# Kernel tuning notes

Measured on AMD Instinct MI355X. Metric: run time of the kernel, lower is better.

## Reference

```python
import jax, jax.numpy as jnp
import numpy as np

H = 1024        # hidden_size
I = 2048        # intermediate_size
E = 8           # num_experts
K = 2           # num_experts_per_tok
AUX_COEF = 0.01
Z_COEF = 0.001


def setup_inputs() -> dict:
    key = jax.random.key(0)
    ks = jax.random.split(key, 8)
    s = 0.02
    return {
        "hidden_states": jax.random.normal(ks[0], (1, 2048, H), dtype=jnp.float32),
        "router_w": jax.random.normal(ks[1], (H, E), dtype=jnp.float32) * s,
        "eg": jax.random.normal(ks[2], (E, H, I), dtype=jnp.float32) * s,  # gate_proj per expert
        "eu": jax.random.normal(ks[3], (E, H, I), dtype=jnp.float32) * s,  # up_proj per expert
        "ed": jax.random.normal(ks[4], (E, I, H), dtype=jnp.float32) * s,  # down_proj per expert
        "sg": jax.random.normal(ks[5], (H, I), dtype=jnp.float32) * s,     # shared expert gate
        "su": jax.random.normal(ks[6], (H, I), dtype=jnp.float32) * s,     # shared expert up
        "sd": jax.random.normal(ks[7], (I, H), dtype=jnp.float32) * s,     # shared expert down
    }


def reference(hidden_states, router_w, eg, eu, ed, sg, su, sd):
    B, S, _ = hidden_states.shape
    x = hidden_states.reshape(-1, H)  # [T, H]

    # shared expert (num_shared_experts = 1)
    shared = (jax.nn.silu(x @ sg) * (x @ su)) @ sd  # [T, H]

    # router: linear -> softmax -> top-k, renormalize top-k probs
    logits = x @ router_w                      # [T, E]
    probs = jax.nn.softmax(logits, axis=-1)
    topw, topi = jax.lax.top_k(probs, K)       # [T, K]
    topw = topw / jnp.sum(topw, axis=-1, keepdims=True)

    # combine weights [T, E]: weight of expert e for token t (0 if not routed)
    combine = jnp.sum(jax.nn.one_hot(topi, E, dtype=x.dtype) * topw[..., None], axis=1)

    # dense expert compute (mathematically identical to masked gather/scatter loop)
    g = jnp.einsum('th,ehi->eti', x, eg)       # [E, T, I]
    u = jnp.einsum('th,ehi->eti', x, eu)
    h = jax.nn.silu(g) * u
    expert_out = jnp.einsum('eti,eih->eth', h, ed)  # [E, T, H]
    routed = jnp.einsum('eth,te->th', expert_out, combine)

    output = (shared + routed).reshape(B, S, H)

    # aux losses: Switch-style load balancing + router z-loss
    f = jnp.mean(jax.nn.one_hot(topi, E, dtype=x.dtype), axis=(0, 1))  # fraction dispatched
    p = jnp.mean(probs, axis=0)                                        # mean router prob
    lb_loss = AUX_COEF * E * jnp.sum(f * p)
    z_loss = Z_COEF * jnp.mean(jax.nn.logsumexp(logits, axis=-1) ** 2)
    aux_loss = lb_loss + z_loss
    return output, aux_loss
```

## Files before the change

### kernel.cpp

```cpp
#include <hip/hip_runtime.h>
#include <hip/hip_bf16.h>
#include <stdint.h>

#define T_ 2048
#define H_ 1024
#define I_ 2048
#define E_ 8
#define NE_ 9

typedef __attribute__((ext_vector_type(8))) short bf16x8;
typedef __attribute__((ext_vector_type(4))) float f32x4;

__device__ __forceinline__ unsigned short f2bf(float f) {
  unsigned int u; __builtin_memcpy(&u, &f, 4);
  u = (u + 0x7fffu + ((u >> 16) & 1u)) >> 16;
  return (unsigned short)u;
}
__device__ __forceinline__ void cvt2(float a, float b, unsigned short* dst) {
  __hip_bfloat162 h = __float22bfloat162_rn(float2{a, b});
  __builtin_memcpy(dst, &h, 4);
}
__device__ __forceinline__ void gll16(const void* g, void* l) {
  __builtin_amdgcn_global_load_lds((const __attribute__((address_space(1))) void*)g,
                                   (__attribute__((address_space(3))) void*)l, 16, 0, 0);
}

__global__ __launch_bounds__(256) void k_pack(
    const float* __restrict__ eg, const float* __restrict__ eu, const float* __restrict__ ed,
    const float* __restrict__ sg, const float* __restrict__ su, const float* __restrict__ sd,
    unsigned short* __restrict__ wgp, unsigned short* __restrict__ wup,
    unsigned short* __restrict__ wdp) {
  int kt = blockIdx.x, nt = blockIdx.y, z = blockIdx.z;
  int grp = z / NE_, e = z % NE_;
  int K = (grp == 2) ? I_ : H_;
  int N = (grp == 2) ? H_ : I_;
  if (kt * 32 >= K || nt * 64 >= N) return;
  const float* src; unsigned short* dst;
  if (grp == 0)      { src = (e < E_) ? eg + (size_t)e * H_ * I_ : sg; dst = wgp + (size_t)e * H_ * I_; }
  else if (grp == 1) { src = (e < E_) ? eu + (size_t)e * H_ * I_ : su; dst = wup + (size_t)e * H_ * I_; }
  else               { src = (e < E_) ? ed + (size_t)e * I_ * H_ : sd; dst = wdp + (size_t)e * I_ * H_; }
  int t = threadIdx.x;
  int q = t >> 6, nn = t & 63;
  int k0 = kt * 32 + q * 8, n = nt * 64 + nn;
  unsigned short o[8];
#pragma unroll
  for (int j = 0; j < 8; j += 2) {
    float a = src[(size_t)(k0 + j) * N + n];
    float b = src[(size_t)(k0 + j + 1) * N + n];
    cvt2(a, b, &o[j]);
  }
  size_t tile = ((size_t)nt * (K / 32) + kt) * 2048;
  *(bf16x8*)&dst[tile + q * 512 + nn * 8] = *(bf16x8*)o;
}

__global__ __launch_bounds__(256) void k_router(
    const float* __restrict__ x, const float* __restrict__ rw,
    int* __restrict__ topi, float* __restrict__ topw,
    float* __restrict__ probs, float* __restrict__ lse2) {
  __shared__ float lrw[E_ * H_];
  int tid = threadIdx.x;
#pragma unroll
  for (int i = 0; i < 8; i++) {
    int idx = i * 256 + tid;
    float4 v = ((const float4*)rw)[idx];
    int f = idx * 4; int h = f >> 3; int e0 = f & 7;
    lrw[(e0 + 0) * H_ + h] = v.x;
    lrw[(e0 + 1) * H_ + h] = v.y;
    lrw[(e0 + 2) * H_ + h] = v.z;
    lrw[(e0 + 3) * H_ + h] = v.w;
  }
  __syncthreads();
  int w = tid >> 6, lane = tid & 63;
  int t = blockIdx.x * 4 + w;
  const float* xp = x + (size_t)t * H_ + lane;
  float xr[16];
#pragma unroll
  for (int j = 0; j < 16; j++) xr[j] = xp[j * 64];
  float acc[E_];
#pragma unroll
  for (int e = 0; e < E_; e++) acc[e] = 0.f;
#pragma unroll
  for (int j = 0; j < 16; j++) {
    float xf = xr[j];
    const float* wp = &lrw[j * 64 + lane];
#pragma unroll
    for (int e = 0; e < E_; e++) acc[e] += xf * wp[e * H_];
  }
#pragma unroll
  for (int off = 32; off >= 1; off >>= 1) {
#pragma unroll
    for (int e = 0; e < E_; e++) acc[e] += __shfl_xor(acc[e], off, 64);
  }
  if (lane == 0) {
    float m = acc[0];
#pragma unroll
    for (int e = 1; e < E_; e++) m = fmaxf(m, acc[e]);
    float p[E_], s = 0.f;
#pragma unroll
    for (int e = 0; e < E_; e++) { p[e] = expf(acc[e] - m); s += p[e]; }
    float inv = 1.f / s;
#pragma unroll
    for (int e = 0; e < E_; e++) p[e] *= inv;
    float lse = m + logf(s);
    lse2[t] = lse * lse;
    float4 p0 = {p[0], p[1], p[2], p[3]}, p1 = {p[4], p[5], p[6], p[7]};
    ((float4*)(probs + t * 8))[0] = p0;
    ((float4*)(probs + t * 8))[1] = p1;
    int i0 = 0;
#pragma unroll
    for (int e = 1; e < E_; e++) if (p[e] > p[i0]) i0 = e;
    int i1 = (i0 == 0) ? 1 : 0;
#pragma unroll
    for (int e = 0; e < E_; e++) if (e != i0 && e != i1 && p[e] > p[i1]) i1 = e;
    float w0 = p[i0], w1 = p[i1], wsum = w0 + w1;
    topi[t * 2] = i0; topi[t * 2 + 1] = i1;
    topw[t * 2] = w0 / wsum; topw[t * 2 + 1] = w1 / wsum;
  }
}

__global__ __launch_bounds__(256) void k_reduce(
    const float* __restrict__ probs, const float* __restrict__ lse2,
    const int* __restrict__ topi,
    int* cnt, int* poffs, float* out_aux) {
  __shared__ float sp[256][9];
  __shared__ int sc[256][8];
  int tid = threadIdx.x;
  float ps[9] = {0.f, 0.f, 0.f, 0.f, 0.f, 0.f, 0.f, 0.f, 0.f};
  int c[8] = {0, 0, 0, 0, 0, 0, 0, 0};
  for (int t = tid; t < T_; t += 256) {
#pragma unroll
    for (int e = 0; e < E_; e++) ps[e] += probs[t * 8 + e];
    ps[8] += lse2[t];
    c[topi[t * 2]]++; c[topi[t * 2 + 1]]++;
  }
#pragma unroll
  for (int e = 0; e < 9; e++) sp[tid][e] = ps[e];
#pragma unroll
  for (int e = 0; e < 8; e++) sc[tid][e] = c[e];
  __syncthreads();
  for (int s = 128; s > 0; s >>= 1) {
    if (tid < s) {
#pragma unroll
      for (int e = 0; e < 9; e++) sp[tid][e] += sp[tid + s][e];
#pragma unroll
      for (int e = 0; e < 8; e++) sc[tid][e] += sc[tid + s][e];
    }
    __syncthreads();
  }
  if (tid == 0) {
#pragma unroll
    for (int e = 0; e < E_; e++) cnt[e] = sc[0][e];
    cnt[E_] = T_;
    int po = 0;
    for (int e = 0; e < NE_; e++) { poffs[e] = po; po += ((cnt[e] + 127) >> 7) << 7; }
    poffs[NE_] = po;
    float lb = 0.f;
#pragma unroll
    for (int e = 0; e < E_; e++)
      lb += ((float)cnt[e] / 4096.f) * (sp[0][e] / 2048.f);
    out_aux[0] = 0.01f * 8.f * lb + 0.001f * (sp[0][8] / 2048.f);
  }
}

__global__ __launch_bounds__(256) void k_fill(
    const int* __restrict__ topi, const float* __restrict__ topw,
    const int* __restrict__ poffs, int* cur, int* tok, float* wgt) {
  __shared__ int hist[8];
  __shared__ int base[8];
  int tid = threadIdx.x;
  int t = blockIdx.x * 256 + tid;
  if (tid < 8) hist[tid] = 0;
  __syncthreads();
  int e0 = topi[t * 2], e1 = topi[t * 2 + 1];
  int p0 = atomicAdd(&hist[e0], 1);
  int p1 = atomicAdd(&hist[e1], 1);
  __syncthreads();
  if (tid < 8) base[tid] = atomicAdd(&cur[tid], hist[tid]);
  __syncthreads();
  tok[poffs[e0] + base[e0] + p0] = t; wgt[poffs[e0] + base[e0] + p0] = topw[t * 2];
  tok[poffs[e1] + base[e1] + p1] = t; wgt[poffs[e1] + base[e1] + p1] = topw[t * 2 + 1];
  int p8 = poffs[E_];
  tok[p8 + t] = t;
  wgt[p8 + t] = 1.f;
}

__global__ __launch_bounds__(256) void k_packA(
    const float* __restrict__ x, const int* __restrict__ cnt,
    const int* __restrict__ poffs, const int* __restrict__ tok,
    unsigned short* __restrict__ apack) {
  int kc = blockIdx.x, mt = blockIdx.y, e = blockIdx.z;
  int cnt_e = cnt[e];
  if (mt * 128 >= cnt_e) return;
  int po = poffs[e];
  int rt = (po >> 7) + mt;
  int t = threadIdx.x;
  int m = t & 127, qh = t >> 7;
  int atok = tok[po + min(mt * 128 + m, cnt_e - 1)];
  const float* arow = x + (size_t)atok * H_;
  size_t abase = (size_t)rt * 32 * 4096;
#pragma unroll
  for (int ki = 0; ki < 4; ki++) {
    int kt = kc * 4 + ki;
#pragma unroll
    for (int qo = 0; qo < 2; qo++) {
      int q = qh + qo * 2;
      const float* s = arow + kt * 32 + q * 8;
      float4 v0 = *(const float4*)s, v1 = *(const float4*)(s + 4);
      unsigned short t8[8];
      cvt2(v0.x, v0.y, t8); cvt2(v0.z, v0.w, t8 + 2);
      cvt2(v1.x, v1.y, t8 + 4); cvt2(v1.z, v1.w, t8 + 6);
      *(bf16x8*)&apack[abase + (size_t)kt * 4096 + q * 1024 + m * 8] = *(bf16x8*)t8;
    }
  }
}

#define G1_GRID 1792
__global__ __launch_bounds__(256) void k_gemm1(
    const unsigned short* __restrict__ apack,
    const unsigned short* __restrict__ wgp, const unsigned short* __restrict__ wup,
    const int* __restrict__ cnt, const int* __restrict__ poffs,
    unsigned short* __restrict__ hbuf) {
  int lin = blockIdx.x;
  int s = (lin & 7) * (G1_GRID / 8) + (lin >> 3);
  int rt = s >> 5, nt = s & 31;
  int rtTotal = poffs[NE_] >> 7;
  if (rt >= rtTotal) return;
  int ro = rt << 7;
  int e = 0;
#pragma unroll
  for (int i = 1; i < NE_; i++) if (poffs[i] <= ro) e = i;
  int po = poffs[e];
  int cnt_e = cnt[e];
  int mt = (ro - po) >> 7;

  __shared__ __align__(16) unsigned short As[2][4096];
  __shared__ __align__(16) unsigned short BgS[2][2048];
  __shared__ __align__(16) unsigned short BuS[2][2048];

  int tid = threadIdx.x;
  int lane = tid & 63, w = tid >> 6;
  int quad = lane >> 4, l15 = lane & 15;
  int wm = w >> 1, wn = w & 1;

  const unsigned short* abase = apack + (size_t)rt * 32 * 4096;
  const unsigned short* bgb = wgp + (size_t)e * H_ * I_ + (size_t)nt * 32 * 2048;
  const unsigned short* bub = wup + (size_t)e * H_ * I_ + (size_t)nt * 32 * 2048;

  f32x4 zero = {0.f, 0.f, 0.f, 0.f};
  f32x4 accg[4][2], accu[4][2];
#pragma unroll
  for (int mi = 0; mi < 4; mi++)
#pragma unroll
    for (int ni = 0; ni < 2; ni++) { accg[mi][ni] = zero; accu[mi][ni] = zero; }

#define STAGE1(kt, b) do { \
    const unsigned short* asrc = abase + (size_t)(kt) * 4096 + w * 1024 + lane * 8; \
    gll16(asrc, &As[b][w * 1024]); \
    gll16(asrc + 512, &As[b][w * 1024 + 512]); \
    gll16(bgb + (size_t)(kt) * 2048 + w * 512 + lane * 8, &BgS[b][w * 512]); \
    gll16(bub + (size_t)(kt) * 2048 + w * 512 + lane * 8, &BuS[b][w * 512]); \
  } while (0)

  STAGE1(0, 0);
  __syncthreads();
  for (int kt = 0; kt < 32; kt++) {
    int cur = kt & 1;
    if (kt < 31) STAGE1(kt + 1, cur ^ 1);
    bf16x8 af[4];
#pragma unroll
    for (int mi = 0; mi < 4; mi++)
      af[mi] = *(const bf16x8*)&As[cur][quad * 1024 + (wm * 64 + mi * 16 + l15) * 8];
#pragma unroll
    for (int ni = 0; ni < 2; ni++) {
      bf16x8 bg = *(const bf16x8*)&BgS[cur][quad * 512 + (wn * 32 + ni * 16 + l15) * 8];
      bf16x8 bu = *(const bf16x8*)&BuS[cur][quad * 512 + (wn * 32 + ni * 16 + l15) * 8];
#pragma unroll
      for (int mi = 0; mi < 4; mi++) {
        accg[mi][ni] = __builtin_amdgcn_mfma_f32_16x16x32_bf16(af[mi], bg, accg[mi][ni], 0, 0, 0);
        accu[mi][ni] = __builtin_amdgcn_mfma_f32_16x16x32_bf16(af[mi], bu, accu[mi][ni], 0, 0, 0);
      }
    }
    __syncthreads();
  }
#undef STAGE1

  size_t hbase = (size_t)rt * 64 * 4096;
  int rem = cnt_e - mt * 128;
#pragma unroll
  for (int ni = 0; ni < 2; ni++) {
    int cc = nt * 64 + wn * 32 + ni * 16 + l15;
    size_t cb = hbase + (size_t)(cc >> 5) * 4096 + (size_t)((cc >> 3) & 3) * 1024 + (cc & 7);
#pragma unroll
    for (int mi = 0; mi < 4; mi++)
#pragma unroll
      for (int r = 0; r < 4; r++) {
        int row = wm * 64 + mi * 16 + quad * 4 + r;
        if (row < rem) {
          float g = accg[mi][ni][r], u = accu[mi][ni][r];
          float sv = g / (1.f + __expf(-g));
          hbuf[cb + (size_t)row * 8] = f2bf(sv * u);
        }
      }
  }
}

#define G2_GRID 896
__global__ __launch_bounds__(256) void k_gemm2(
    const unsigned short* __restrict__ hbuf, const unsigned short* __restrict__ wdp,
    const int* __restrict__ cnt, const int* __restrict__ poffs,
    const int* __restrict__ tok, const float* __restrict__ wgt,
    float* __restrict__ out) {
  int lin = blockIdx.x;
  int s = (lin & 7) * (G2_GRID / 8) + (lin >> 3);
  int rt = s >> 4;
  int r4 = s & 15;
  int nt = r4 >> 1, kh = r4 & 1;
  int rtTotal = poffs[NE_] >> 7;
  if (rt >= rtTotal) return;
  int ro = rt << 7;
  int e = 0;
#pragma unroll
  for (int i = 1; i < NE_; i++) if (poffs[i] <= ro) e = i;
  int po = poffs[e];
  int cnt_e = cnt[e];
  int mt = (ro - po) >> 7;

  __shared__ __align__(16) unsigned short As[2][4096];
  __shared__ __align__(16) unsigned short BdS[2][4096];

  int tid = threadIdx.x;
  int lane = tid & 63, w = tid >> 6;
  int quad = lane >> 4, l15 = lane & 15;
  int wm = w >> 1, wn = w & 1;

  const unsigned short* abase = hbuf + (size_t)rt * 64 * 4096;
  const unsigned short* bb0 = wdp + (size_t)e * I_ * H_ + ((size_t)(2 * nt) * 64) * 2048;
  const unsigned short* bb1 = wdp + (size_t)e * I_ * H_ + ((size_t)(2 * nt + 1) * 64) * 2048;

  f32x4 zero = {0.f, 0.f, 0.f, 0.f};
  f32x4 acc[4][4];
#pragma unroll
  for (int mi = 0; mi < 4; mi++)
#pragma unroll
    for (int ni = 0; ni < 4; ni++) acc[mi][ni] = zero;

#define STAGE2(kt, b) do { \
    const unsigned short* asrc = abase + (size_t)(kt) * 4096 + w * 1024 + lane * 8; \
    gll16(asrc, &As[b][w * 1024]); \
    gll16(asrc + 512, &As[b][w * 1024 + 512]); \
    gll16(bb0 + (size_t)(kt) * 2048 + w * 512 + lane * 8, &BdS[b][w * 512]); \
    gll16(bb1 + (size_t)(kt) * 2048 + w * 512 + lane * 8, &BdS[b][2048 + w * 512]); \
  } while (0)

  int k0 = kh * 32;
  STAGE2(k0, 0);
  __syncthreads();
  for (int kk = 0; kk < 32; kk++) {
    int cur = kk & 1;
    if (kk < 31) STAGE2(k0 + kk + 1, cur ^ 1);
    bf16x8 af[4];
#pragma unroll
    for (int mi = 0; mi < 4; mi++)
      af[mi] = *(const bf16x8*)&As[cur][quad * 1024 + (wm * 64 + mi * 16 + l15) * 8];
#pragma unroll
    for (int ni = 0; ni < 4; ni++) {
      bf16x8 bd = *(const bf16x8*)&BdS[cur][wn * 2048 + quad * 512 + (ni * 16 + l15) * 8];
#pragma unroll
      for (int mi = 0; mi < 4; mi++)
        acc[mi][ni] = __builtin_amdgcn_mfma_f32_16x16x32_bf16(af[mi], bd, acc[mi][ni], 0, 0, 0);
    }
    __syncthreads();
  }
#undef STAGE2

  int rem = cnt_e - mt * 128;
#pragma unroll
  for (int mi = 0; mi < 4; mi++)
#pragma unroll
    for (int r = 0; r < 4; r++) {
      int row = wm * 64 + mi * 16 + quad * 4 + r;
      if (row < rem) {
        int g = po + mt * 128 + row;
        int tt = tok[g];
        float wt = wgt[g];
#pragma unroll
        for (int ni = 0; ni < 4; ni++) {
          int col = nt * 128 + wn * 64 + ni * 16 + l15;
          atomicAdd(&out[(size_t)tt * H_ + col], wt * acc[mi][ni][r]);
        }
      }
    }
}

extern "C" void kernel_launch(void* const* d_in, const int* in_sizes, int n_in,
                              void* d_out, int out_size, void* d_ws, size_t ws_size,
                              hipStream_t stream) {
  const float* x  = (const float*)d_in[0];
  const float* rw = (const float*)d_in[1];
  const float* eg = (const float*)d_in[2];
  const float* eu = (const float*)d_in[3];
  const float* ed = (const float*)d_in[4];
  const float* sg = (const float*)d_in[5];
  const float* su = (const float*)d_in[6];
  const float* sd = (const float*)d_in[7];
  float* out = (float*)d_out;
  char* ws = (char*)d_ws;

  int*   cnt  = (int*)(ws + 64);
  int*   poffs= (int*)(ws + 128);
  int*   cur  = (int*)(ws + 256);
  int*   topi = (int*)(ws + 4096);
  float* topw = (float*)(ws + 4096 + 16384);
  int*   tok  = (int*)(ws + 36864);
  float* wgt  = (float*)(ws + 66560);
  unsigned short* apack = (unsigned short*)(ws + 131072);
  unsigned short* hbuf  = (unsigned short*)(ws + 131072 + 14811136);
  float* probs = (float*)(ws + 44302336);
  float* lse2  = (float*)(ws + 44367872);
  unsigned short* wgp   = (unsigned short*)(ws + 131072 + 14811136 + 29491200);
  unsigned short* wup   = (unsigned short*)((char*)wgp + (size_t)NE_ * H_ * I_ * 2);
  unsigned short* wdp   = (unsigned short*)((char*)wup + (size_t)NE_ * H_ * I_ * 2);

  hipMemsetAsync(ws, 0, 4096, stream);
  hipMemsetAsync(out, 0, (size_t)T_ * H_ * 4, stream);

  dim3 gp(64, 32, 3 * NE_);
  k_pack<<<gp, 256, 0, stream>>>(eg, eu, ed, sg, su, sd, wgp, wup, wdp);
  k_router<<<512, 256, 0, stream>>>(x, rw, topi, topw, probs, lse2);
  k_reduce<<<1, 256, 0, stream>>>(probs, lse2, topi, cnt, poffs, out + (size_t)T_ * H_);
  k_fill<<<8, 256, 0, stream>>>(topi, topw, poffs, cur, tok, wgt);
  dim3 ga(8, 16, NE_);
  k_packA<<<ga, 256, 0, stream>>>(x, cnt, poffs, tok, apack);
  k_gemm1<<<G1_GRID, 256, 0, stream>>>(apack, wgp, wup, cnt, poffs, hbuf);
  k_gemm2<<<G2_GRID, 256, 0, stream>>>(hbuf, wdp, cnt, poffs, tok, wgt, out);
}
```

Before: 428.0 us.

## Fuse pre-GEMM kernels, drop memsets, and coalesce weight pack via LDS

The router kernel now zeroes the output buffer, which replaces both memsets. Reduce and fill are merged into one single-block scheduling kernel that builds the token lists with shared-memory atomics. Weight packing and activation packing are merged into one prep kernel. The weight transpose now reads coalesced float4 rows through an LDS tile instead of strided scalar loads. The goal is fewer launches and better memory coalescing in the weight conversion that dominates pre-GEMM traffic. The cost is a serial single-block fill loop over all tokens.

```diff
diff --git a/kernel.cpp b/kernel.cpp
--- a/kernel.cpp
+++ b/kernel.cpp
@@ -25,40 +25,19 @@
                                    (__attribute__((address_space(3))) void*)l, 16, 0, 0);
 }
 
-__global__ __launch_bounds__(256) void k_pack(
-    const float* __restrict__ eg, const float* __restrict__ eu, const float* __restrict__ ed,
-    const float* __restrict__ sg, const float* __restrict__ su, const float* __restrict__ sd,
-    unsigned short* __restrict__ wgp, unsigned short* __restrict__ wup,
-    unsigned short* __restrict__ wdp) {
-  int kt = blockIdx.x, nt = blockIdx.y, z = blockIdx.z;
-  int grp = z / NE_, e = z % NE_;
-  int K = (grp == 2) ? I_ : H_;
-  int N = (grp == 2) ? H_ : I_;
-  if (kt * 32 >= K || nt * 64 >= N) return;
-  const float* src; unsigned short* dst;
-  if (grp == 0)      { src = (e < E_) ? eg + (size_t)e * H_ * I_ : sg; dst = wgp + (size_t)e * H_ * I_; }
-  else if (grp == 1) { src = (e < E_) ? eu + (size_t)e * H_ * I_ : su; dst = wup + (size_t)e * H_ * I_; }
-  else               { src = (e < E_) ? ed + (size_t)e * I_ * H_ : sd; dst = wdp + (size_t)e * I_ * H_; }
-  int t = threadIdx.x;
-  int q = t >> 6, nn = t & 63;
-  int k0 = kt * 32 + q * 8, n = nt * 64 + nn;
-  unsigned short o[8];
-#pragma unroll
-  for (int j = 0; j < 8; j += 2) {
-    float a = src[(size_t)(k0 + j) * N + n];
-    float b = src[(size_t)(k0 + j + 1) * N + n];
-    cvt2(a, b, &o[j]);
-  }
-  size_t tile = ((size_t)nt * (K / 32) + kt) * 2048;
-  *(bf16x8*)&dst[tile + q * 512 + nn * 8] = *(bf16x8*)o;
-}
-
 __global__ __launch_bounds__(256) void k_router(
     const float* __restrict__ x, const float* __restrict__ rw,
     int* __restrict__ topi, float* __restrict__ topw,
-    float* __restrict__ probs, float* __restrict__ lse2) {
+    float* __restrict__ probs, float* __restrict__ lse2,
+    float* __restrict__ outz) {
+  int tid = threadIdx.x;
+  {
+    float4 zf = {0.f, 0.f, 0.f, 0.f};
+    float4* ob = (float4*)(outz + (size_t)blockIdx.x * 4096);
+#pragma unroll
+    for (int i = 0; i < 4; i++) ob[i * 256 + tid] = zf;
+  }
   __shared__ float lrw[E_ * H_];
-  int tid = threadIdx.x;
 #pragma unroll
   for (int i = 0; i < 8; i++) {
     int idx = i * 256 + tid;
@@ -118,12 +97,15 @@
   }
 }
 
-__global__ __launch_bounds__(256) void k_reduce(
+__global__ __launch_bounds__(256) void k_sched(
     const float* __restrict__ probs, const float* __restrict__ lse2,
-    const int* __restrict__ topi,
-    int* cnt, int* poffs, float* out_aux) {
+    const int* __restrict__ topi, const float* __restrict__ topw,
+    int* cnt, int* poffs, float* out_aux,
+    int* __restrict__ tok, float* __restrict__ wgt) {
   __shared__ float sp[256][9];
   __shared__ int sc[256][8];
+  __shared__ int sbase[NE_];
+  __shared__ int scur[8];
   int tid = threadIdx.x;
   float ps[9] = {0.f, 0.f, 0.f, 0.f, 0.f, 0.f, 0.f, 0.f, 0.f};
   int c[8] = {0, 0, 0, 0, 0, 0, 0, 0};
@@ -152,64 +134,96 @@
     for (int e = 0; e < E_; e++) cnt[e] = sc[0][e];
     cnt[E_] = T_;
     int po = 0;
-    for (int e = 0; e < NE_; e++) { poffs[e] = po; po += ((cnt[e] + 127) >> 7) << 7; }
+    for (int e = 0; e < NE_; e++) {
+      poffs[e] = po; sbase[e] = po;
+      int ce = (e < E_) ? sc[0][e] : T_;
+      po += ((ce + 127) >> 7) << 7;
+    }
     poffs[NE_] = po;
     float lb = 0.f;
 #pragma unroll
     for (int e = 0; e < E_; e++)
-      lb += ((float)cnt[e] / 4096.f) * (sp[0][e] / 2048.f);
+      lb += ((float)sc[0][e] / 4096.f) * (sp[0][e] / 2048.f);
     out_aux[0] = 0.01f * 8.f * lb + 0.001f * (sp[0][8] / 2048.f);
   }
-}
-
-__global__ __launch_bounds__(256) void k_fill(
-    const int* __restrict__ topi, const float* __restrict__ topw,
-    const int* __restrict__ poffs, int* cur, int* tok, float* wgt) {
-  __shared__ int hist[8];
-  __shared__ int base[8];
-  int tid = threadIdx.x;
-  int t = blockIdx.x * 256 + tid;
-  if (tid < 8) hist[tid] = 0;
+  if (tid < 8) scur[tid] = 0;
   __syncthreads();
-  int e0 = topi[t * 2], e1 = topi[t * 2 + 1];
-  int p0 = atomicAdd(&hist[e0], 1);
-  int p1 = atomicAdd(&hist[e1], 1);
-  __syncthreads();
-  if (tid < 8) base[tid] = atomicAdd(&cur[tid], hist[tid]);
-  __syncthreads();
-  tok[poffs[e0] + base[e0] + p0] = t; wgt[poffs[e0] + base[e0] + p0] = topw[t * 2];
-  tok[poffs[e1] + base[e1] + p1] = t; wgt[poffs[e1] + base[e1] + p1] = topw[t * 2 + 1];
-  int p8 = poffs[E_];
-  tok[p8 + t] = t;
-  wgt[p8 + t] = 1.f;
-}
-
-__global__ __launch_bounds__(256) void k_packA(
+  for (int t = tid; t < T_; t += 256) {
+    int e0 = topi[t * 2], e1 = topi[t * 2 + 1];
+    int p0 = atomicAdd(&scur[e0], 1);
+    int p1 = atomicAdd(&scur[e1], 1);
+    tok[sbase[e0] + p0] = t; wgt[sbase[e0] + p0] = topw[t * 2];
+    tok[sbase[e1] + p1] = t; wgt[sbase[e1] + p1] = topw[t * 2 + 1];
+    tok[sbase[E_] + t] = t; wgt[sbase[E_] + t] = 1.f;
+  }
+}
+
+#define PACK_BLKS 27648
+#define PREP_GRID 28800
+__global__ __launch_bounds__(256) void k_prep(
+    const float* __restrict__ eg, const float* __restrict__ eu, const float* __restrict__ ed,
+    const float* __restrict__ sg, const float* __restrict__ su, const float* __restrict__ sd,
+    unsigned short* __restrict__ wgp, unsigned short* __restrict__ wup,
+    unsigned short* __restrict__ wdp,
     const float* __restrict__ x, const int* __restrict__ cnt,
     const int* __restrict__ poffs, const int* __restrict__ tok,
     unsigned short* __restrict__ apack) {
-  int kc = blockIdx.x, mt = blockIdx.y, e = blockIdx.z;
-  int cnt_e = cnt[e];
-  if (mt * 128 >= cnt_e) return;
-  int po = poffs[e];
-  int rt = (po >> 7) + mt;
+  __shared__ __align__(16) float lds[32 * 68];
+  int bz = blockIdx.x;
   int t = threadIdx.x;
-  int m = t & 127, qh = t >> 7;
-  int atok = tok[po + min(mt * 128 + m, cnt_e - 1)];
-  const float* arow = x + (size_t)atok * H_;
-  size_t abase = (size_t)rt * 32 * 4096;
-#pragma unroll
-  for (int ki = 0; ki < 4; ki++) {
-    int kt = kc * 4 + ki;
-#pragma unroll
-    for (int qo = 0; qo < 2; qo++) {
-      int q = qh + qo * 2;
-      const float* s = arow + kt * 32 + q * 8;
-      float4 v0 = *(const float4*)s, v1 = *(const float4*)(s + 4);
-      unsigned short t8[8];
-      cvt2(v0.x, v0.y, t8); cvt2(v0.z, v0.w, t8 + 2);
-      cvt2(v1.x, v1.y, t8 + 4); cvt2(v1.z, v1.w, t8 + 6);
-      *(bf16x8*)&apack[abase + (size_t)kt * 4096 + q * 1024 + m * 8] = *(bf16x8*)t8;
+  if (bz < PACK_BLKS) {
+    int mat = bz >> 10, tile = bz & 1023;
+    int grp = mat / NE_, e = mat % NE_;
+    int K, N, kt, nt;
+    if (grp == 2) { K = I_; N = H_; kt = tile >> 4; nt = tile & 15; }
+    else          { K = H_; N = I_; kt = tile >> 5; nt = tile & 31; }
+    const float* src; unsigned short* dst;
+    if (grp == 0)      { src = (e < E_) ? eg + (size_t)e * H_ * I_ : sg; dst = wgp + (size_t)e * H_ * I_; }
+    else if (grp == 1) { src = (e < E_) ? eu + (size_t)e * H_ * I_ : su; dst = wup + (size_t)e * H_ * I_; }
+    else               { src = (e < E_) ? ed + (size_t)e * I_ * H_ : sd; dst = wdp + (size_t)e * I_ * H_; }
+
+    const float* srcbase = src + (size_t)(kt * 32) * N + nt * 64;
+    int r0 = t >> 4, c0 = (t & 15) * 4;
+    float4 v0 = *(const float4*)(srcbase + (size_t)r0 * N + c0);
+    float4 v1 = *(const float4*)(srcbase + (size_t)(r0 + 16) * N + c0);
+    *(float4*)&lds[r0 * 68 + c0] = v0;
+    *(float4*)&lds[(r0 + 16) * 68 + c0] = v1;
+    __syncthreads();
+
+    int q = t >> 6, nn = t & 63;
+    unsigned short o[8];
+#pragma unroll
+    for (int j = 0; j < 8; j += 2) {
+      float a = lds[(q * 8 + j) * 68 + nn];
+      float b = lds[(q * 8 + j + 1) * 68 + nn];
+      cvt2(a, b, &o[j]);
+    }
+    size_t tile_off = ((size_t)nt * (K / 32) + kt) * 2048;
+    *(bf16x8*)&dst[tile_off + q * 512 + nn * 8] = *(bf16x8*)o;
+  } else {
+    int id = bz - PACK_BLKS;
+    int kc = id & 7, mt = (id >> 3) & 15, e = id >> 7;
+    int cnt_e = cnt[e];
+    if (mt * 128 >= cnt_e) return;
+    int po = poffs[e];
+    int rt = (po >> 7) + mt;
+    int m = t & 127, qh = t >> 7;
+    int atok = tok[po + min(mt * 128 + m, cnt_e - 1)];
+    const float* arow = x + (size_t)atok * H_;
+    size_t abase = (size_t)rt * 32 * 4096;
+#pragma unroll
+    for (int ki = 0; ki < 4; ki++) {
+      int kt = kc * 4 + ki;
+#pragma unroll
+      for (int qo = 0; qo < 2; qo++) {
+        int q = qh + qo * 2;
+        const float* s = arow + kt * 32 + q * 8;
+        float4 v0 = *(const float4*)s, v1 = *(const float4*)(s + 4);
+        unsigned short t8[8];
+        cvt2(v0.x, v0.y, t8); cvt2(v0.z, v0.w, t8 + 2);
+        cvt2(v1.x, v1.y, t8 + 4); cvt2(v1.z, v1.w, t8 + 6);
+        *(bf16x8*)&apack[abase + (size_t)kt * 4096 + q * 1024 + m * 8] = *(bf16x8*)t8;
+      }
     }
   }
 }
@@ -408,7 +422,6 @@
 
   int*   cnt  = (int*)(ws + 64);
   int*   poffs= (int*)(ws + 128);
-  int*   cur  = (int*)(ws + 256);
   int*   topi = (int*)(ws + 4096);
   float* topw = (float*)(ws + 4096 + 16384);
   int*   tok  = (int*)(ws + 36864);
@@ -421,16 +434,11 @@
   unsigned short* wup   = (unsigned short*)((char*)wgp + (size_t)NE_ * H_ * I_ * 2);
   unsigned short* wdp   = (unsigned short*)((char*)wup + (size_t)NE_ * H_ * I_ * 2);
 
-  hipMemsetAsync(ws, 0, 4096, stream);
-  hipMemsetAsync(out, 0, (size_t)T_ * H_ * 4, stream);
-
-  dim3 gp(64, 32, 3 * NE_);
-  k_pack<<<gp, 256, 0, stream>>>(eg, eu, ed, sg, su, sd, wgp, wup, wdp);
-  k_router<<<512, 256, 0, stream>>>(x, rw, topi, topw, probs, lse2);
-  k_reduce<<<1, 256, 0, stream>>>(probs, lse2, topi, cnt, poffs, out + (size_t)T_ * H_);
-  k_fill<<<8, 256, 0, stream>>>(topi, topw, poffs, cur, tok, wgt);
-  dim3 ga(8, 16, NE_);
-  k_packA<<<ga, 256, 0, stream>>>(x, cnt, poffs, tok, apack);
+  k_router<<<512, 256, 0, stream>>>(x, rw, topi, topw, probs, lse2, out);
+  k_sched<<<1, 256, 0, stream>>>(probs, lse2, topi, topw, cnt, poffs,
+                                 out + (size_t)T_ * H_, tok, wgt);
+  k_prep<<<PREP_GRID, 256, 0, stream>>>(eg, eu, ed, sg, su, sd, wgp, wup, wdp,
+                                        x, cnt, poffs, tok, apack);
   k_gemm1<<<G1_GRID, 256, 0, stream>>>(apack, wgp, wup, cnt, poffs, hbuf);
   k_gemm2<<<G2_GRID, 256, 0, stream>>>(hbuf, wdp, cnt, poffs, tok, wgt, out);
 }
```

New measurement: 426.4 us. Within noise of the previous version (-0.4%).
